# Kernel optimization log

Measured on AMD Instinct MI355X. Metric: run time of the kernel, lower is better.

## Reference

```python
import jax, jax.numpy as jnp
import numpy as np

N, H, S = 100, 16, 6  # n_subactors, neurons, state_size
B, T = 128, 128


def setup_inputs() -> dict:
    key = jax.random.key(0)
    ks = jax.random.split(key, 12)
    sc = 1.0 / np.sqrt(H)
    inp = {
        "x":   jax.random.normal(ks[0], (B, T, N, S), dtype=jnp.float32),
        # stacked per-subactor GRU weights (torch gate order: r, z, n)
        "Wih": jax.random.uniform(ks[1], (N, 3 * H, S), minval=-sc, maxval=sc, dtype=jnp.float32),
        "Whh": jax.random.uniform(ks[2], (N, 3 * H, H), minval=-sc, maxval=sc, dtype=jnp.float32),
        "bih": jax.random.uniform(ks[3], (N, 3 * H), minval=-sc, maxval=sc, dtype=jnp.float32),
        "bhh": jax.random.uniform(ks[4], (N, 3 * H), minval=-sc, maxval=sc, dtype=jnp.float32),
        # stacked per-subactor MLP weights
        "W1": jax.random.uniform(ks[5], (N, H, H), minval=-sc, maxval=sc, dtype=jnp.float32),
        "b1": jax.random.uniform(ks[6], (N, H), minval=-sc, maxval=sc, dtype=jnp.float32),
        "W2": jax.random.uniform(ks[7], (N, H, H), minval=-sc, maxval=sc, dtype=jnp.float32),
        "b2": jax.random.uniform(ks[8], (N, H), minval=-sc, maxval=sc, dtype=jnp.float32),
        "W3": jax.random.uniform(ks[9], (N, 1, H), minval=-sc, maxval=sc, dtype=jnp.float32),
        "b3": jax.random.uniform(ks[10], (N, 1), minval=-sc, maxval=sc, dtype=jnp.float32),
    }
    return inp


def reference(x, Wih, Whh, bih, bhh, W1, b1, W2, b2, W3, b3):
    b, t, n, s = x.shape
    h = Whh.shape[-1]
    # input projections for all timesteps/subactors at once: [B,T,N,3H]
    xi = jnp.einsum('btns,ngs->btng', x, Wih) + bih

    def step(hprev, xt):  # hprev [B,N,H], xt [B,N,3H]
        hh = jnp.einsum('bnh,ngh->bng', hprev, Whh) + bhh
        xr, xz, xn = jnp.split(xt, 3, axis=-1)
        hr, hz, hn = jnp.split(hh, 3, axis=-1)
        r = jax.nn.sigmoid(xr + hr)
        z = jax.nn.sigmoid(xz + hz)
        nn_ = jnp.tanh(xn + r * hn)
        hnew = (1.0 - z) * nn_ + z * hprev
        return hnew, hnew

    h0 = jnp.zeros((b, n, h), dtype=x.dtype)
    _, hs = jax.lax.scan(step, h0, jnp.moveaxis(xi, 1, 0))  # [T,B,N,H]
    hs = jnp.moveaxis(hs, 0, 1)  # [B,T,N,H]

    y = jax.nn.relu(jnp.einsum('btnh,nkh->btnk', hs, W1) + b1)
    y = jax.nn.relu(jnp.einsum('btnh,nkh->btnk', y, W2) + b2)
    y = jax.nn.relu(jnp.einsum('btnh,nkh->btnk', y, W3) + b3)  # [B,T,N,1]
    # torch: stack over subactors -> [N,B,T,1] then .view(-1, t, nzones)
    return jnp.transpose(y, (2, 0, 1, 3)).reshape(-1, t, n)
```

## Files before the change

kernel.cpp:

```cpp
#include <hip/hip_runtime.h>

namespace {

constexpr int kN = 100;
constexpr int kH = 16;
constexpr int kS = 6;
constexpr int kB = 128;
constexpr int kT = 128;
constexpr int kNS = kN * kS;
constexpr int kXB = kT * kNS;
constexpr float kL2E = 1.44269504088896340736f;

typedef float f32x4 __attribute__((ext_vector_type(4)));
typedef float vf2 __attribute__((ext_vector_type(2)));
typedef short bf16x8 __attribute__((ext_vector_type(8)));

union Frag {
  unsigned u[4];
  bf16x8 v;
};

__device__ __forceinline__ unsigned pkbf(float a, float b) {
  unsigned ua = __builtin_bit_cast(unsigned, a);
  unsigned ub = __builtin_bit_cast(unsigned, b);
  ua += 0x7fffu + ((ua >> 16) & 1u);
  ub += 0x7fffu + ((ub >> 16) & 1u);
  return (ua >> 16) | (ub & 0xffff0000u);
}

__device__ __forceinline__ float rcp_fast(float v) {
  return __builtin_amdgcn_rcpf(v);
}
__device__ __forceinline__ float exp2_fast(float v) {
  return __builtin_amdgcn_exp2f(v);
}
__device__ __forceinline__ vf2 pkfma(vf2 a, vf2 b, vf2 c) {
  return __builtin_elementwise_fma(a, b, c);
}

__device__ __forceinline__ f32x4 mfma16(bf16x8 a, bf16x8 b, f32x4 c) {
  return __builtin_amdgcn_mfma_f32_16x16x32_bf16(a, b, c, 0, 0, 0);
}

__device__ __forceinline__ void mkA(Frag& F, int qt, const float* hrow,
                                    const float* xrow, float sc) {
  F.u[0] = F.u[1] = F.u[2] = F.u[3] = 0u;
  if (hrow) {
    F.u[0] = pkbf(hrow[4 * qt + 0] * sc, hrow[4 * qt + 1] * sc);
    F.u[1] = pkbf(hrow[4 * qt + 2] * sc, hrow[4 * qt + 3] * sc);
  }
  if (xrow && qt < 3) {
    F.u[2] = pkbf(xrow[2 * qt + 0] * sc, xrow[2 * qt + 1] * sc);
  }
}

}

__global__ __launch_bounds__(64) void actor_db(
    const float* __restrict__ x, const float* __restrict__ Wih,
    const float* __restrict__ Whh, const float* __restrict__ bih,
    const float* __restrict__ bhh, const float* __restrict__ W1,
    const float* __restrict__ b1, const float* __restrict__ W2,
    const float* __restrict__ b2, const float* __restrict__ W3,
    const float* __restrict__ b3, float* __restrict__ out) {
  const int tid = (int)threadIdx.x;
  const int j = tid & 15;
  const int qt = tid >> 4;
  const int n = (int)blockIdx.x >> 3;
  const int bt = (int)blockIdx.x & 7;

  Frag Ar, Az, Anh, Anx, Ay1, Ay2;
  mkA(Ar, qt, Whh + ((size_t)n * 48 + j) * 16, Wih + ((size_t)n * 48 + j) * 6,
      kL2E);
  mkA(Az, qt, Whh + ((size_t)n * 48 + 16 + j) * 16,
      Wih + ((size_t)n * 48 + 16 + j) * 6, kL2E);
  mkA(Anh, qt, Whh + ((size_t)n * 48 + 32 + j) * 16, nullptr, 2.0f * kL2E);
  mkA(Anx, qt, nullptr, Wih + ((size_t)n * 48 + 32 + j) * 6, 2.0f * kL2E);
  mkA(Ay1, qt, W1 + ((size_t)n * 16 + j) * 16, nullptr, 1.0f);
  mkA(Ay2, qt, W2 + ((size_t)n * 16 + j) * 16, nullptr, 1.0f);

  f32x4 Cbr, Cbz, Cbhn, Cbin, Cb1, Cb2;
  vf2 w301, w323;
#pragma unroll
  for (int r = 0; r < 4; ++r) {
    const int gi = n * 48 + 4 * qt + r;
    Cbr[r] = (bih[gi] + bhh[gi]) * kL2E;
    Cbz[r] = (bih[gi + 16] + bhh[gi + 16]) * kL2E;
    Cbin[r] = bih[gi + 32] * 2.0f * kL2E;
    Cbhn[r] = bhh[gi + 32] * 2.0f * kL2E;
    const int hi = n * 16 + 4 * qt + r;
    Cb1[r] = b1[hi];
    Cb2[r] = b2[hi];
  }
  w301 = (vf2){W3[n * 16 + 4 * qt + 0], W3[n * 16 + 4 * qt + 1]};
  w323 = (vf2){W3[n * 16 + 4 * qt + 2], W3[n * 16 + 4 * qt + 3]};
  const float b3s = b3[n];

  const int b = bt * 16 + j;
  const float* px =
      x + (size_t)b * kXB + (size_t)n * kS + (qt < 3 ? 2 * qt : 0);
  float* outp = out + ((size_t)n * kB + b) * kT;

  float2 xa[4], xb[4];
#pragma unroll
  for (int i = 0; i < 4; ++i) {
    xa[i] = *(const float2*)(px + (size_t)i * kNS);
    xb[i] = *(const float2*)(px + (size_t)(i + 4) * kNS);
  }

  vf2 hp01 = (vf2){0.f, 0.f}, hp23 = (vf2){0.f, 0.f};
  unsigned P0 = 0u, P1 = 0u;

  const f32x4 zero4 = {0.f, 0.f, 0.f, 0.f};
  f32x4 Cy1p = zero4;
  f32x4 Cy2p = zero4;
  float s4[4] = {0.f, 0.f, 0.f, 0.f};

  const vf2 one2 = (vf2){1.f, 1.f};
  const vf2 m2 = (vf2){-2.f, -2.f};
  const vf2 z2 = (vf2){0.f, 0.f};

  auto step = [&](int t, float2 xv, bool doRec, bool doA, bool doB,
                  bool doC) {
    f32x4 Cr, Cz, Chn, Cxn, Cy1n = Cy1p;
    if (t <= kT) {
      Frag Bf;
      Bf.u[0] = P0;
      Bf.u[1] = P1;
      Bf.u[2] = pkbf(xv.x, xv.y);
      Bf.u[3] = 0u;
      if (doRec) {
        Cr = mfma16(Ar.v, Bf.v, Cbr);
        Cz = mfma16(Az.v, Bf.v, Cbz);
        Chn = mfma16(Anh.v, Bf.v, Cbhn);
        Cxn = mfma16(Anx.v, Bf.v, Cbin);
      }
      Cy1n = mfma16(Ay1.v, Bf.v, Cb1);
    }

    if (doB) {
      vf2 a = __builtin_elementwise_max((vf2){Cy2p[0], Cy2p[1]}, z2);
      vf2 c = __builtin_elementwise_max((vf2){Cy2p[2], Cy2p[3]}, z2);
      vf2 p = pkfma(c, w323, a * w301);
      s4[(t - 3) & 3] = p.x + p.y;
    }

    if (doA) {
      vf2 a = __builtin_elementwise_max((vf2){Cy1p[0], Cy1p[1]}, z2);
      vf2 c = __builtin_elementwise_max((vf2){Cy1p[2], Cy1p[3]}, z2);
      Frag By;
      By.u[0] = pkbf(a.x, a.y);
      By.u[1] = pkbf(c.x, c.y);
      By.u[2] = 0u;
      By.u[3] = 0u;
      Cy2p = mfma16(Ay2.v, By.v, Cb2);
    }

    if (doC) {
      float v0 = s4[0], v1 = s4[1], v2 = s4[2], v3 = s4[3];
      v0 += __shfl_xor(v0, 16);
      v1 += __shfl_xor(v1, 16);
      v2 += __shfl_xor(v2, 16);
      v3 += __shfl_xor(v3, 16);
      v0 += __shfl_xor(v0, 32);
      v1 += __shfl_xor(v1, 32);
      v2 += __shfl_xor(v2, 32);
      v3 += __shfl_xor(v3, 32);
      if (qt == 0) {
        float4 o = {fmaxf(v0 + b3s, 0.f), fmaxf(v1 + b3s, 0.f),
                    fmaxf(v2 + b3s, 0.f), fmaxf(v3 + b3s, 0.f)};
        *(float4*)(outp + (t - 6)) = o;
      }
    }

    if (doRec) {
      vf2 cr01 = {Cr[0], Cr[1]}, cr23 = {Cr[2], Cr[3]};
      vf2 cz01 = {Cz[0], Cz[1]}, cz23 = {Cz[2], Cz[3]};
      vf2 chn01 = {Chn[0], Chn[1]}, chn23 = {Chn[2], Chn[3]};
      vf2 cxn01 = {Cxn[0], Cxn[1]}, cxn23 = {Cxn[2], Cxn[3]};

      vf2 er01 = {exp2_fast(-cr01.x), exp2_fast(-cr01.y)};
      vf2 er23 = {exp2_fast(-cr23.x), exp2_fast(-cr23.y)};
      vf2 dr01 = er01 + one2, dr23 = er23 + one2;
      vf2 rr01 = {rcp_fast(dr01.x), rcp_fast(dr01.y)};
      vf2 rr23 = {rcp_fast(dr23.x), rcp_fast(dr23.y)};

      vf2 ez01 = {exp2_fast(-cz01.x), exp2_fast(-cz01.y)};
      vf2 ez23 = {exp2_fast(-cz23.x), exp2_fast(-cz23.y)};
      vf2 dz01 = ez01 + one2, dz23 = ez23 + one2;
      vf2 zz01 = {rcp_fast(dz01.x), rcp_fast(dz01.y)};
      vf2 zz23 = {rcp_fast(dz23.x), rcp_fast(dz23.y)};

      vf2 np01 = pkfma(rr01, chn01, cxn01);
      vf2 np23 = pkfma(rr23, chn23, cxn23);
      vf2 en01 = {exp2_fast(np01.x), exp2_fast(np01.y)};
      vf2 en23 = {exp2_fast(np23.x), exp2_fast(np23.y)};
      vf2 dn01 = en01 + one2, dn23 = en23 + one2;
      vf2 rn01 = {rcp_fast(dn01.x), rcp_fast(dn01.y)};
      vf2 rn23 = {rcp_fast(dn23.x), rcp_fast(dn23.y)};
      vf2 nn01 = pkfma(m2, rn01, one2);
      vf2 nn23 = pkfma(m2, rn23, one2);

      hp01 = pkfma(zz01, hp01 - nn01, nn01);
      hp23 = pkfma(zz23, hp23 - nn23, nn23);
      P0 = pkbf(hp01.x, hp01.y);
      P1 = pkbf(hp23.x, hp23.y);
    }

    Cy1p = Cy1n;
  };

  for (int t8 = 0; t8 < kT; t8 += 8) {
    const bool p0 = (t8 > 0);
    step(t8 + 0, xa[0], true, p0 || false, p0, false);
    step(t8 + 1, xa[1], true, true, p0, false);
    step(t8 + 2, xa[2], true, true, true, p0);
    step(t8 + 3, xa[3], true, true, true, false);
#pragma unroll
    for (int i = 0; i < 4; ++i) {
      int tc = t8 + 8 + i;
      if (tc > kT - 1) tc = kT - 1;
      xa[i] = *(const float2*)(px + (size_t)tc * kNS);
    }
    step(t8 + 4, xb[0], true, true, true, false);
    step(t8 + 5, xb[1], true, true, true, false);
    step(t8 + 6, xb[2], true, true, true, true);
    step(t8 + 7, xb[3], true, true, true, false);
#pragma unroll
    for (int i = 0; i < 4; ++i) {
      int tc = t8 + 12 + i;
      if (tc > kT - 1) tc = kT - 1;
      xb[i] = *(const float2*)(px + (size_t)tc * kNS);
    }
  }

  const float2 xz = {0.f, 0.f};
  step(kT, xz, false, true, true, false);
  step(kT + 1, xz, false, true, true, false);
  step(kT + 2, xz, false, false, true, true);
}

extern "C" void kernel_launch(void* const* d_in, const int* in_sizes, int n_in,
                              void* d_out, int out_size, void* d_ws,
                              size_t ws_size, hipStream_t stream) {
  const float* x = (const float*)d_in[0];
  const float* Wih = (const float*)d_in[1];
  const float* Whh = (const float*)d_in[2];
  const float* bih = (const float*)d_in[3];
  const float* bhh = (const float*)d_in[4];
  const float* W1 = (const float*)d_in[5];
  const float* b1 = (const float*)d_in[6];
  const float* W2 = (const float*)d_in[7];
  const float* b2 = (const float*)d_in[8];
  const float* W3 = (const float*)d_in[9];
  const float* b3 = (const float*)d_in[10];
  float* out = (float*)d_out;

  actor_db<<<dim3(kN * 8), dim3(64), 0, stream>>>(x, Wih, Whh, bih, bhh, W1,
                                                  b1, W2, b2, W3, b3, out);
}
```

Measured before the change: 135.0 us.

## Split GRU gate nonlinearities across two wavefronts with LDS hidden-state exchange

Each block now runs two wavefronts. Both issue the recurrent MFMAs redundantly, and each evaluates the sigmoid/tanh gate math for only half of the four accumulator rows. The updated bf16 hidden halves are exchanged through double-buffered shared memory with a __syncthreads every timestep, and the MLP head runs only on wave 0. This halves the serial transcendental chain per wave on the recurrence critical path, at the cost of a block barrier and an LDS round trip per step plus duplicated MFMA work.

```diff
diff --git a/kernel.cpp b/kernel.cpp
--- a/kernel.cpp
+++ b/kernel.cpp
@@ -56,7 +56,7 @@
 
 }
 
-__global__ __launch_bounds__(64) void actor_db(
+__global__ __launch_bounds__(128, 1) void actor_r17(
     const float* __restrict__ x, const float* __restrict__ Wih,
     const float* __restrict__ Whh, const float* __restrict__ bih,
     const float* __restrict__ bhh, const float* __restrict__ W1,
@@ -64,10 +64,14 @@
     const float* __restrict__ b2, const float* __restrict__ W3,
     const float* __restrict__ b3, float* __restrict__ out) {
   const int tid = (int)threadIdx.x;
-  const int j = tid & 15;
-  const int qt = tid >> 4;
+  const int w = tid >> 6;
+  const int lane = tid & 63;
+  const int j = lane & 15;
+  const int qt = lane >> 4;
   const int n = (int)blockIdx.x >> 3;
   const int bt = (int)blockIdx.x & 7;
+
+  __shared__ unsigned Lx[2][2][64];
 
   Frag Ar, Az, Anh, Anx, Ay1, Ay2;
   mkA(Ar, qt, Whh + ((size_t)n * 48 + j) * 16, Wih + ((size_t)n * 48 + j) * 6,
@@ -108,7 +112,7 @@
     xb[i] = *(const float2*)(px + (size_t)(i + 4) * kNS);
   }
 
-  vf2 hp01 = (vf2){0.f, 0.f}, hp23 = (vf2){0.f, 0.f};
+  vf2 hpH = (vf2){0.f, 0.f};
   unsigned P0 = 0u, P1 = 0u;
 
   const f32x4 zero4 = {0.f, 0.f, 0.f, 0.f};
@@ -122,6 +126,7 @@
 
   auto step = [&](int t, float2 xv, bool doRec, bool doA, bool doB,
                   bool doC) {
+    const int par = t & 1;
     f32x4 Cr, Cz, Chn, Cxn, Cy1n = Cy1p;
     if (t <= kT) {
       Frag Bf;
@@ -135,17 +140,17 @@
         Chn = mfma16(Anh.v, Bf.v, Cbhn);
         Cxn = mfma16(Anx.v, Bf.v, Cbin);
       }
-      Cy1n = mfma16(Ay1.v, Bf.v, Cb1);
-    }
-
-    if (doB) {
+      if (w == 0) Cy1n = mfma16(Ay1.v, Bf.v, Cb1);
+    }
+
+    if (w == 0 && doB) {
       vf2 a = __builtin_elementwise_max((vf2){Cy2p[0], Cy2p[1]}, z2);
       vf2 c = __builtin_elementwise_max((vf2){Cy2p[2], Cy2p[3]}, z2);
       vf2 p = pkfma(c, w323, a * w301);
       s4[(t - 3) & 3] = p.x + p.y;
     }
 
-    if (doA) {
+    if (w == 0 && doA) {
       vf2 a = __builtin_elementwise_max((vf2){Cy1p[0], Cy1p[1]}, z2);
       vf2 c = __builtin_elementwise_max((vf2){Cy1p[2], Cy1p[3]}, z2);
       Frag By;
@@ -156,55 +161,68 @@
       Cy2p = mfma16(Ay2.v, By.v, Cb2);
     }
 
-    if (doC) {
-      float v0 = s4[0], v1 = s4[1], v2 = s4[2], v3 = s4[3];
-      v0 += __shfl_xor(v0, 16);
-      v1 += __shfl_xor(v1, 16);
-      v2 += __shfl_xor(v2, 16);
-      v3 += __shfl_xor(v3, 16);
-      v0 += __shfl_xor(v0, 32);
-      v1 += __shfl_xor(v1, 32);
-      v2 += __shfl_xor(v2, 32);
-      v3 += __shfl_xor(v3, 32);
-      if (qt == 0) {
-        float4 o = {fmaxf(v0 + b3s, 0.f), fmaxf(v1 + b3s, 0.f),
-                    fmaxf(v2 + b3s, 0.f), fmaxf(v3 + b3s, 0.f)};
-        *(float4*)(outp + (t - 6)) = o;
+    if (doRec) {
+      vf2 crH = w ? (vf2){Cr[2], Cr[3]} : (vf2){Cr[0], Cr[1]};
+      vf2 czH = w ? (vf2){Cz[2], Cz[3]} : (vf2){Cz[0], Cz[1]};
+      vf2 chnH = w ? (vf2){Chn[2], Chn[3]} : (vf2){Chn[0], Chn[1]};
+      vf2 cxnH = w ? (vf2){Cxn[2], Cxn[3]} : (vf2){Cxn[0], Cxn[1]};
+
+      vf2 erH = {exp2_fast(-crH.x), exp2_fast(-crH.y)};
+      vf2 ezH = {exp2_fast(-czH.x), exp2_fast(-czH.y)};
+      vf2 drH = erH + one2;
+      vf2 rrH = {rcp_fast(drH.x), rcp_fast(drH.y)};
+      vf2 dzH = ezH + one2;
+      vf2 zzH = {rcp_fast(dzH.x), rcp_fast(dzH.y)};
+
+      vf2 npH = pkfma(rrH, chnH, cxnH);
+      vf2 enH = {exp2_fast(npH.x), exp2_fast(npH.y)};
+      vf2 dnH = enH + one2;
+      vf2 rnH = {rcp_fast(dnH.x), rcp_fast(dnH.y)};
+      vf2 nnH = pkfma(m2, rnH, one2);
+
+      hpH = pkfma(zzH, hpH - nnH, nnH);
+      const unsigned Pm = pkbf(hpH.x, hpH.y);
+
+      Lx[par][w][lane] = Pm;
+      __syncthreads();
+      const unsigned Po = Lx[par][w ^ 1][lane];
+
+      if (w == 0 && doC) {
+        float v0 = s4[0], v1 = s4[1], v2 = s4[2], v3 = s4[3];
+        v0 += __shfl_xor(v0, 16);
+        v1 += __shfl_xor(v1, 16);
+        v2 += __shfl_xor(v2, 16);
+        v3 += __shfl_xor(v3, 16);
+        v0 += __shfl_xor(v0, 32);
+        v1 += __shfl_xor(v1, 32);
+        v2 += __shfl_xor(v2, 32);
+        v3 += __shfl_xor(v3, 32);
+        if (qt == 0) {
+          float4 o = {fmaxf(v0 + b3s, 0.f), fmaxf(v1 + b3s, 0.f),
+                      fmaxf(v2 + b3s, 0.f), fmaxf(v3 + b3s, 0.f)};
+          *(float4*)(outp + (t - 6)) = o;
+        }
       }
-    }
-
-    if (doRec) {
-      vf2 cr01 = {Cr[0], Cr[1]}, cr23 = {Cr[2], Cr[3]};
-      vf2 cz01 = {Cz[0], Cz[1]}, cz23 = {Cz[2], Cz[3]};
-      vf2 chn01 = {Chn[0], Chn[1]}, chn23 = {Chn[2], Chn[3]};
-      vf2 cxn01 = {Cxn[0], Cxn[1]}, cxn23 = {Cxn[2], Cxn[3]};
-
-      vf2 er01 = {exp2_fast(-cr01.x), exp2_fast(-cr01.y)};
-      vf2 er23 = {exp2_fast(-cr23.x), exp2_fast(-cr23.y)};
-      vf2 dr01 = er01 + one2, dr23 = er23 + one2;
-      vf2 rr01 = {rcp_fast(dr01.x), rcp_fast(dr01.y)};
-      vf2 rr23 = {rcp_fast(dr23.x), rcp_fast(dr23.y)};
-
-      vf2 ez01 = {exp2_fast(-cz01.x), exp2_fast(-cz01.y)};
-      vf2 ez23 = {exp2_fast(-cz23.x), exp2_fast(-cz23.y)};
-      vf2 dz01 = ez01 + one2, dz23 = ez23 + one2;
-      vf2 zz01 = {rcp_fast(dz01.x), rcp_fast(dz01.y)};
-      vf2 zz23 = {rcp_fast(dz23.x), rcp_fast(dz23.y)};
-
-      vf2 np01 = pkfma(rr01, chn01, cxn01);
-      vf2 np23 = pkfma(rr23, chn23, cxn23);
-      vf2 en01 = {exp2_fast(np01.x), exp2_fast(np01.y)};
-      vf2 en23 = {exp2_fast(np23.x), exp2_fast(np23.y)};
-      vf2 dn01 = en01 + one2, dn23 = en23 + one2;
-      vf2 rn01 = {rcp_fast(dn01.x), rcp_fast(dn01.y)};
-      vf2 rn23 = {rcp_fast(dn23.x), rcp_fast(dn23.y)};
-      vf2 nn01 = pkfma(m2, rn01, one2);
-      vf2 nn23 = pkfma(m2, rn23, one2);
-
-      hp01 = pkfma(zz01, hp01 - nn01, nn01);
-      hp23 = pkfma(zz23, hp23 - nn23, nn23);
-      P0 = pkbf(hp01.x, hp01.y);
-      P1 = pkbf(hp23.x, hp23.y);
+
+      P0 = w ? Po : Pm;
+      P1 = w ? Pm : Po;
+    } else {
+      if (w == 0 && doC) {
+        float v0 = s4[0], v1 = s4[1], v2 = s4[2], v3 = s4[3];
+        v0 += __shfl_xor(v0, 16);
+        v1 += __shfl_xor(v1, 16);
+        v2 += __shfl_xor(v2, 16);
+        v3 += __shfl_xor(v3, 16);
+        v0 += __shfl_xor(v0, 32);
+        v1 += __shfl_xor(v1, 32);
+        v2 += __shfl_xor(v2, 32);
+        v3 += __shfl_xor(v3, 32);
+        if (qt == 0) {
+          float4 o = {fmaxf(v0 + b3s, 0.f), fmaxf(v1 + b3s, 0.f),
+                      fmaxf(v2 + b3s, 0.f), fmaxf(v3 + b3s, 0.f)};
+          *(float4*)(outp + (t - 6)) = o;
+        }
+      }
     }
 
     Cy1p = Cy1n;
@@ -212,7 +230,7 @@
 
   for (int t8 = 0; t8 < kT; t8 += 8) {
     const bool p0 = (t8 > 0);
-    step(t8 + 0, xa[0], true, p0 || false, p0, false);
+    step(t8 + 0, xa[0], true, p0, p0, false);
     step(t8 + 1, xa[1], true, true, p0, false);
     step(t8 + 2, xa[2], true, true, true, p0);
     step(t8 + 3, xa[3], true, true, true, false);
@@ -256,6 +274,6 @@
   const float* b3 = (const float*)d_in[10];
   float* out = (float*)d_out;
 
-  actor_db<<<dim3(kN * 8), dim3(64), 0, stream>>>(x, Wih, Whh, bih, bhh, W1,
-                                                  b1, W2, b2, W3, b3, out);
-}
+  actor_r17<<<dim3(kN * 8), dim3(128), 0, stream>>>(x, Wih, Whh, bih, bhh, W1,
+                                                    b1, W2, b2, W3, b3, out);
+}
```

Result: slower. 156.6 us (+16.0%).

## Interleave two independent batch tiles per wavefront to hide recurrence latency

Applied to the files above, without the earlier changes.

Each wavefront now processes two independent 16-batch tiles (A and B) of the same subactor, interleaving their MFMA and transcendental chains. The grid drops from 800 to 400 single-wave blocks. The intent is to hide the serial MFMA→exp→rcp dependency latency of the GRU recurrence through instruction-level parallelism, at the cost of more registers per thread and fewer blocks in flight across the CUs.

```diff
diff --git a/kernel.cpp b/kernel.cpp
--- a/kernel.cpp
+++ b/kernel.cpp
@@ -56,7 +56,7 @@
 
 }
 
-__global__ __launch_bounds__(64) void actor_db(
+__global__ __launch_bounds__(64, 1) void actor_r23(
     const float* __restrict__ x, const float* __restrict__ Wih,
     const float* __restrict__ Whh, const float* __restrict__ bih,
     const float* __restrict__ bhh, const float* __restrict__ W1,
@@ -66,8 +66,8 @@
   const int tid = (int)threadIdx.x;
   const int j = tid & 15;
   const int qt = tid >> 4;
-  const int n = (int)blockIdx.x >> 3;
-  const int bt = (int)blockIdx.x & 7;
+  const int n = (int)blockIdx.x >> 2;
+  const int pr = (int)blockIdx.x & 3;
 
   Frag Ar, Az, Anh, Anx, Ay1, Ay2;
   mkA(Ar, qt, Whh + ((size_t)n * 48 + j) * 16, Wih + ((size_t)n * 48 + j) * 6,
@@ -96,148 +96,219 @@
   w323 = (vf2){W3[n * 16 + 4 * qt + 2], W3[n * 16 + 4 * qt + 3]};
   const float b3s = b3[n];
 
-  const int b = bt * 16 + j;
-  const float* px =
-      x + (size_t)b * kXB + (size_t)n * kS + (qt < 3 ? 2 * qt : 0);
-  float* outp = out + ((size_t)n * kB + b) * kT;
-
-  float2 xa[4], xb[4];
+  const int bA = (2 * pr + 0) * 16 + j;
+  const int bB = (2 * pr + 1) * 16 + j;
+  const int qoff = (qt < 3 ? 2 * qt : 0);
+  const float* pxA = x + (size_t)bA * kXB + (size_t)n * kS + qoff;
+  const float* pxB = x + (size_t)bB * kXB + (size_t)n * kS + qoff;
+  float* outpA = out + ((size_t)n * kB + bA) * kT;
+  float* outpB = out + ((size_t)n * kB + bB) * kT;
+
+  float2 xaA[4], xbA[4], xaB[4], xbB[4];
 #pragma unroll
   for (int i = 0; i < 4; ++i) {
-    xa[i] = *(const float2*)(px + (size_t)i * kNS);
-    xb[i] = *(const float2*)(px + (size_t)(i + 4) * kNS);
-  }
-
-  vf2 hp01 = (vf2){0.f, 0.f}, hp23 = (vf2){0.f, 0.f};
-  unsigned P0 = 0u, P1 = 0u;
+    xaA[i] = *(const float2*)(pxA + (size_t)i * kNS);
+    xbA[i] = *(const float2*)(pxA + (size_t)(i + 4) * kNS);
+    xaB[i] = *(const float2*)(pxB + (size_t)i * kNS);
+    xbB[i] = *(const float2*)(pxB + (size_t)(i + 4) * kNS);
+  }
+
+  vf2 hp01A = (vf2){0.f, 0.f}, hp23A = (vf2){0.f, 0.f};
+  vf2 hp01B = (vf2){0.f, 0.f}, hp23B = (vf2){0.f, 0.f};
+  unsigned P0A = 0u, P1A = 0u, P0B = 0u, P1B = 0u;
 
   const f32x4 zero4 = {0.f, 0.f, 0.f, 0.f};
-  f32x4 Cy1p = zero4;
-  f32x4 Cy2p = zero4;
-  float s4[4] = {0.f, 0.f, 0.f, 0.f};
+  f32x4 Cy1pA = zero4, Cy2pA = zero4;
+  f32x4 Cy1pB = zero4, Cy2pB = zero4;
+  float s4A[4] = {0.f, 0.f, 0.f, 0.f};
+  float s4B[4] = {0.f, 0.f, 0.f, 0.f};
 
   const vf2 one2 = (vf2){1.f, 1.f};
   const vf2 m2 = (vf2){-2.f, -2.f};
   const vf2 z2 = (vf2){0.f, 0.f};
 
-  auto step = [&](int t, float2 xv, bool doRec, bool doA, bool doB,
-                  bool doC) {
-    f32x4 Cr, Cz, Chn, Cxn, Cy1n = Cy1p;
+  auto step = [&](int t, float2 xvA, float2 xvB, bool doRec, bool doA,
+                  bool doB_, bool doC) {
+    f32x4 CrA, CzA, ChnA, CxnA, Cy1nA = Cy1pA;
+    f32x4 CrB, CzB, ChnB, CxnB, Cy1nB = Cy1pB;
     if (t <= kT) {
-      Frag Bf;
-      Bf.u[0] = P0;
-      Bf.u[1] = P1;
-      Bf.u[2] = pkbf(xv.x, xv.y);
-      Bf.u[3] = 0u;
+      Frag BfA, BfB;
+      BfA.u[0] = P0A;
+      BfA.u[1] = P1A;
+      BfA.u[2] = pkbf(xvA.x, xvA.y);
+      BfA.u[3] = 0u;
+      BfB.u[0] = P0B;
+      BfB.u[1] = P1B;
+      BfB.u[2] = pkbf(xvB.x, xvB.y);
+      BfB.u[3] = 0u;
       if (doRec) {
-        Cr = mfma16(Ar.v, Bf.v, Cbr);
-        Cz = mfma16(Az.v, Bf.v, Cbz);
-        Chn = mfma16(Anh.v, Bf.v, Cbhn);
-        Cxn = mfma16(Anx.v, Bf.v, Cbin);
+        CrA = mfma16(Ar.v, BfA.v, Cbr);
+        CrB = mfma16(Ar.v, BfB.v, Cbr);
+        CzA = mfma16(Az.v, BfA.v, Cbz);
+        CzB = mfma16(Az.v, BfB.v, Cbz);
+        ChnA = mfma16(Anh.v, BfA.v, Cbhn);
+        ChnB = mfma16(Anh.v, BfB.v, Cbhn);
+        CxnA = mfma16(Anx.v, BfA.v, Cbin);
+        CxnB = mfma16(Anx.v, BfB.v, Cbin);
       }
-      Cy1n = mfma16(Ay1.v, Bf.v, Cb1);
-    }
-
-    if (doB) {
-      vf2 a = __builtin_elementwise_max((vf2){Cy2p[0], Cy2p[1]}, z2);
-      vf2 c = __builtin_elementwise_max((vf2){Cy2p[2], Cy2p[3]}, z2);
-      vf2 p = pkfma(c, w323, a * w301);
-      s4[(t - 3) & 3] = p.x + p.y;
+      Cy1nA = mfma16(Ay1.v, BfA.v, Cb1);
+      Cy1nB = mfma16(Ay1.v, BfB.v, Cb1);
+    }
+
+    if (doB_) {
+      vf2 aA = __builtin_elementwise_max((vf2){Cy2pA[0], Cy2pA[1]}, z2);
+      vf2 cA = __builtin_elementwise_max((vf2){Cy2pA[2], Cy2pA[3]}, z2);
+      vf2 aB = __builtin_elementwise_max((vf2){Cy2pB[0], Cy2pB[1]}, z2);
+      vf2 cB = __builtin_elementwise_max((vf2){Cy2pB[2], Cy2pB[3]}, z2);
+      vf2 pA = pkfma(cA, w323, aA * w301);
+      vf2 pB = pkfma(cB, w323, aB * w301);
+      s4A[(t - 3) & 3] = pA.x + pA.y;
+      s4B[(t - 3) & 3] = pB.x + pB.y;
     }
 
     if (doA) {
-      vf2 a = __builtin_elementwise_max((vf2){Cy1p[0], Cy1p[1]}, z2);
-      vf2 c = __builtin_elementwise_max((vf2){Cy1p[2], Cy1p[3]}, z2);
-      Frag By;
-      By.u[0] = pkbf(a.x, a.y);
-      By.u[1] = pkbf(c.x, c.y);
-      By.u[2] = 0u;
-      By.u[3] = 0u;
-      Cy2p = mfma16(Ay2.v, By.v, Cb2);
+      vf2 aA = __builtin_elementwise_max((vf2){Cy1pA[0], Cy1pA[1]}, z2);
+      vf2 cA = __builtin_elementwise_max((vf2){Cy1pA[2], Cy1pA[3]}, z2);
+      vf2 aB = __builtin_elementwise_max((vf2){Cy1pB[0], Cy1pB[1]}, z2);
+      vf2 cB = __builtin_elementwise_max((vf2){Cy1pB[2], Cy1pB[3]}, z2);
+      Frag ByA, ByB;
+      ByA.u[0] = pkbf(aA.x, aA.y);
+      ByA.u[1] = pkbf(cA.x, cA.y);
+      ByA.u[2] = 0u;
+      ByA.u[3] = 0u;
+      ByB.u[0] = pkbf(aB.x, aB.y);
+      ByB.u[1] = pkbf(cB.x, cB.y);
+      ByB.u[2] = 0u;
+      ByB.u[3] = 0u;
+      Cy2pA = mfma16(Ay2.v, ByA.v, Cb2);
+      Cy2pB = mfma16(Ay2.v, ByB.v, Cb2);
     }
 
     if (doC) {
-      float v0 = s4[0], v1 = s4[1], v2 = s4[2], v3 = s4[3];
-      v0 += __shfl_xor(v0, 16);
-      v1 += __shfl_xor(v1, 16);
-      v2 += __shfl_xor(v2, 16);
-      v3 += __shfl_xor(v3, 16);
-      v0 += __shfl_xor(v0, 32);
-      v1 += __shfl_xor(v1, 32);
-      v2 += __shfl_xor(v2, 32);
-      v3 += __shfl_xor(v3, 32);
+      float a0 = s4A[0], a1 = s4A[1], a2 = s4A[2], a3 = s4A[3];
+      float b0 = s4B[0], b1v = s4B[1], b2v = s4B[2], b3v = s4B[3];
+      a0 += __shfl_xor(a0, 16);
+      a1 += __shfl_xor(a1, 16);
+      a2 += __shfl_xor(a2, 16);
+      a3 += __shfl_xor(a3, 16);
+      b0 += __shfl_xor(b0, 16);
+      b1v += __shfl_xor(b1v, 16);
+      b2v += __shfl_xor(b2v, 16);
+      b3v += __shfl_xor(b3v, 16);
+      a0 += __shfl_xor(a0, 32);
+      a1 += __shfl_xor(a1, 32);
+      a2 += __shfl_xor(a2, 32);
+      a3 += __shfl_xor(a3, 32);
+      b0 += __shfl_xor(b0, 32);
+      b1v += __shfl_xor(b1v, 32);
+      b2v += __shfl_xor(b2v, 32);
+      b3v += __shfl_xor(b3v, 32);
       if (qt == 0) {
-        float4 o = {fmaxf(v0 + b3s, 0.f), fmaxf(v1 + b3s, 0.f),
-                    fmaxf(v2 + b3s, 0.f), fmaxf(v3 + b3s, 0.f)};
-        *(float4*)(outp + (t - 6)) = o;
+        float4 oA = {fmaxf(a0 + b3s, 0.f), fmaxf(a1 + b3s, 0.f),
+                     fmaxf(a2 + b3s, 0.f), fmaxf(a3 + b3s, 0.f)};
+        float4 oB = {fmaxf(b0 + b3s, 0.f), fmaxf(b1v + b3s, 0.f),
+                     fmaxf(b2v + b3s, 0.f), fmaxf(b3v + b3s, 0.f)};
+        *(float4*)(outpA + (t - 6)) = oA;
+        *(float4*)(outpB + (t - 6)) = oB;
       }
     }
 
     if (doRec) {
-      vf2 cr01 = {Cr[0], Cr[1]}, cr23 = {Cr[2], Cr[3]};
-      vf2 cz01 = {Cz[0], Cz[1]}, cz23 = {Cz[2], Cz[3]};
-      vf2 chn01 = {Chn[0], Chn[1]}, chn23 = {Chn[2], Chn[3]};
-      vf2 cxn01 = {Cxn[0], Cxn[1]}, cxn23 = {Cxn[2], Cxn[3]};
-
-      vf2 er01 = {exp2_fast(-cr01.x), exp2_fast(-cr01.y)};
-      vf2 er23 = {exp2_fast(-cr23.x), exp2_fast(-cr23.y)};
-      vf2 dr01 = er01 + one2, dr23 = er23 + one2;
-      vf2 rr01 = {rcp_fast(dr01.x), rcp_fast(dr01.y)};
-      vf2 rr23 = {rcp_fast(dr23.x), rcp_fast(dr23.y)};
-
-      vf2 ez01 = {exp2_fast(-cz01.x), exp2_fast(-cz01.y)};
-      vf2 ez23 = {exp2_fast(-cz23.x), exp2_fast(-cz23.y)};
-      vf2 dz01 = ez01 + one2, dz23 = ez23 + one2;
-      vf2 zz01 = {rcp_fast(dz01.x), rcp_fast(dz01.y)};
-      vf2 zz23 = {rcp_fast(dz23.x), rcp_fast(dz23.y)};
-
-      vf2 np01 = pkfma(rr01, chn01, cxn01);
-      vf2 np23 = pkfma(rr23, chn23, cxn23);
-      vf2 en01 = {exp2_fast(np01.x), exp2_fast(np01.y)};
-      vf2 en23 = {exp2_fast(np23.x), exp2_fast(np23.y)};
-      vf2 dn01 = en01 + one2, dn23 = en23 + one2;
-      vf2 rn01 = {rcp_fast(dn01.x), rcp_fast(dn01.y)};
-      vf2 rn23 = {rcp_fast(dn23.x), rcp_fast(dn23.y)};
-      vf2 nn01 = pkfma(m2, rn01, one2);
-      vf2 nn23 = pkfma(m2, rn23, one2);
-
-      hp01 = pkfma(zz01, hp01 - nn01, nn01);
-      hp23 = pkfma(zz23, hp23 - nn23, nn23);
-      P0 = pkbf(hp01.x, hp01.y);
-      P1 = pkbf(hp23.x, hp23.y);
-    }
-
-    Cy1p = Cy1n;
+      vf2 cr01A = {CrA[0], CrA[1]}, cr23A = {CrA[2], CrA[3]};
+      vf2 cz01A = {CzA[0], CzA[1]}, cz23A = {CzA[2], CzA[3]};
+      vf2 cr01B = {CrB[0], CrB[1]}, cr23B = {CrB[2], CrB[3]};
+      vf2 cz01B = {CzB[0], CzB[1]}, cz23B = {CzB[2], CzB[3]};
+      vf2 chn01A = {ChnA[0], ChnA[1]}, chn23A = {ChnA[2], ChnA[3]};
+      vf2 cxn01A = {CxnA[0], CxnA[1]}, cxn23A = {CxnA[2], CxnA[3]};
+      vf2 chn01B = {ChnB[0], ChnB[1]}, chn23B = {ChnB[2], ChnB[3]};
+      vf2 cxn01B = {CxnB[0], CxnB[1]}, cxn23B = {CxnB[2], CxnB[3]};
+
+      vf2 er01A = {exp2_fast(-cr01A.x), exp2_fast(-cr01A.y)};
+      vf2 er23A = {exp2_fast(-cr23A.x), exp2_fast(-cr23A.y)};
+      vf2 er01B = {exp2_fast(-cr01B.x), exp2_fast(-cr01B.y)};
+      vf2 er23B = {exp2_fast(-cr23B.x), exp2_fast(-cr23B.y)};
+      vf2 ez01A = {exp2_fast(-cz01A.x), exp2_fast(-cz01A.y)};
+      vf2 ez23A = {exp2_fast(-cz23A.x), exp2_fast(-cz23A.y)};
+      vf2 ez01B = {exp2_fast(-cz01B.x), exp2_fast(-cz01B.y)};
+      vf2 ez23B = {exp2_fast(-cz23B.x), exp2_fast(-cz23B.y)};
+
+      vf2 dr01A = er01A + one2, dr23A = er23A + one2;
+      vf2 dr01B = er01B + one2, dr23B = er23B + one2;
+      vf2 rr01A = {rcp_fast(dr01A.x), rcp_fast(dr01A.y)};
+      vf2 rr23A = {rcp_fast(dr23A.x), rcp_fast(dr23A.y)};
+      vf2 rr01B = {rcp_fast(dr01B.x), rcp_fast(dr01B.y)};
+      vf2 rr23B = {rcp_fast(dr23B.x), rcp_fast(dr23B.y)};
+
+      vf2 dz01A = ez01A + one2, dz23A = ez23A + one2;
+      vf2 dz01B = ez01B + one2, dz23B = ez23B + one2;
+      vf2 zz01A = {rcp_fast(dz01A.x), rcp_fast(dz01A.y)};
+      vf2 zz23A = {rcp_fast(dz23A.x), rcp_fast(dz23A.y)};
+      vf2 zz01B = {rcp_fast(dz01B.x), rcp_fast(dz01B.y)};
+      vf2 zz23B = {rcp_fast(dz23B.x), rcp_fast(dz23B.y)};
+
+      vf2 np01A = pkfma(rr01A, chn01A, cxn01A);
+      vf2 np23A = pkfma(rr23A, chn23A, cxn23A);
+      vf2 np01B = pkfma(rr01B, chn01B, cxn01B);
+      vf2 np23B = pkfma(rr23B, chn23B, cxn23B);
+      vf2 en01A = {exp2_fast(np01A.x), exp2_fast(np01A.y)};
+      vf2 en23A = {exp2_fast(np23A.x), exp2_fast(np23A.y)};
+      vf2 en01B = {exp2_fast(np01B.x), exp2_fast(np01B.y)};
+      vf2 en23B = {exp2_fast(np23B.x), exp2_fast(np23B.y)};
+      vf2 dn01A = en01A + one2, dn23A = en23A + one2;
+      vf2 dn01B = en01B + one2, dn23B = en23B + one2;
+      vf2 rn01A = {rcp_fast(dn01A.x), rcp_fast(dn01A.y)};
+      vf2 rn23A = {rcp_fast(dn23A.x), rcp_fast(dn23A.y)};
+      vf2 rn01B = {rcp_fast(dn01B.x), rcp_fast(dn01B.y)};
+      vf2 rn23B = {rcp_fast(dn23B.x), rcp_fast(dn23B.y)};
+      vf2 nn01A = pkfma(m2, rn01A, one2);
+      vf2 nn23A = pkfma(m2, rn23A, one2);
+      vf2 nn01B = pkfma(m2, rn01B, one2);
+      vf2 nn23B = pkfma(m2, rn23B, one2);
+
+      hp01A = pkfma(zz01A, hp01A - nn01A, nn01A);
+      hp23A = pkfma(zz23A, hp23A - nn23A, nn23A);
+      hp01B = pkfma(zz01B, hp01B - nn01B, nn01B);
+      hp23B = pkfma(zz23B, hp23B - nn23B, nn23B);
+      P0A = pkbf(hp01A.x, hp01A.y);
+      P1A = pkbf(hp23A.x, hp23A.y);
+      P0B = pkbf(hp01B.x, hp01B.y);
+      P1B = pkbf(hp23B.x, hp23B.y);
+    }
+
+    Cy1pA = Cy1nA;
+    Cy1pB = Cy1nB;
   };
 
   for (int t8 = 0; t8 < kT; t8 += 8) {
     const bool p0 = (t8 > 0);
-    step(t8 + 0, xa[0], true, p0 || false, p0, false);
-    step(t8 + 1, xa[1], true, true, p0, false);
-    step(t8 + 2, xa[2], true, true, true, p0);
-    step(t8 + 3, xa[3], true, true, true, false);
+    step(t8 + 0, xaA[0], xaB[0], true, p0, p0, false);
+    step(t8 + 1, xaA[1], xaB[1], true, true, p0, false);
+    step(t8 + 2, xaA[2], xaB[2], true, true, true, p0);
+    step(t8 + 3, xaA[3], xaB[3], true, true, true, false);
 #pragma unroll
     for (int i = 0; i < 4; ++i) {
       int tc = t8 + 8 + i;
       if (tc > kT - 1) tc = kT - 1;
-      xa[i] = *(const float2*)(px + (size_t)tc * kNS);
-    }
-    step(t8 + 4, xb[0], true, true, true, false);
-    step(t8 + 5, xb[1], true, true, true, false);
-    step(t8 + 6, xb[2], true, true, true, true);
-    step(t8 + 7, xb[3], true, true, true, false);
+      xaA[i] = *(const float2*)(pxA + (size_t)tc * kNS);
+      xaB[i] = *(const float2*)(pxB + (size_t)tc * kNS);
+    }
+    step(t8 + 4, xbA[0], xbB[0], true, true, true, false);
+    step(t8 + 5, xbA[1], xbB[1], true, true, true, false);
+    step(t8 + 6, xbA[2], xbB[2], true, true, true, true);
+    step(t8 + 7, xbA[3], xbB[3], true, true, true, false);
 #pragma unroll
     for (int i = 0; i < 4; ++i) {
       int tc = t8 + 12 + i;
       if (tc > kT - 1) tc = kT - 1;
-      xb[i] = *(const float2*)(px + (size_t)tc * kNS);
+      xbA[i] = *(const float2*)(pxA + (size_t)tc * kNS);
+      xbB[i] = *(const float2*)(pxB + (size_t)tc * kNS);
     }
   }
 
   const float2 xz = {0.f, 0.f};
-  step(kT, xz, false, true, true, false);
-  step(kT + 1, xz, false, true, true, false);
-  step(kT + 2, xz, false, false, true, true);
+  step(kT, xz, xz, false, true, true, false);
+  step(kT + 1, xz, xz, false, true, true, false);
+  step(kT + 2, xz, xz, false, false, true, true);
 }
 
 extern "C" void kernel_launch(void* const* d_in, const int* in_sizes, int n_in,
@@ -256,6 +327,6 @@
   const float* b3 = (const float*)d_in[10];
   float* out = (float*)d_out;
 
-  actor_db<<<dim3(kN * 8), dim3(64), 0, stream>>>(x, Wih, Whh, bih, bhh, W1,
-                                                  b1, W2, b2, W3, b3, out);
-}
+  actor_r23<<<dim3(kN * 4), dim3(64), 0, stream>>>(x, Wih, Whh, bih, bhh, W1,
+                                                   b1, W2, b2, W3, b3, out);
+}
```

Measured after the change: 168.1 us. 24.5% more time.
